# Kernel tuning notes

Hardware: AMD Instinct MI355X
Metric: run time of the kernel (lower is better)

Reference implementation:

```python
import jax, jax.numpy as jnp
import numpy as np

EMB_TABLE = 80000  # full shared embedding rows
N_ITEMS = 50000    # target item count (item_num + 1)
E = 600000         # edges
D = 128            # embedding_size
L = 3              # num_gcn_layers


def gcn_conv(x, W, b, src, dst, norm, n):
    # PyG GCNConv: x' = lin(x); out[i] = sum_{(j->i)} norm_ji * x'[j] + bias
    msgs = (x @ W)[src] * norm[:, None]          # [E+n, D]
    out = jax.ops.segment_sum(msgs, dst, num_segments=n)
    return out + b


def setup_inputs() -> dict:
    key = jax.random.key(0)
    k0, k1, k2 = jax.random.split(key, 3)
    item_emb = jax.random.normal(k0, (EMB_TABLE, D), dtype=jnp.float32) * 0.02
    weights = jax.random.normal(k1, (L, D, D), dtype=jnp.float32) * (1.0 / np.sqrt(D))
    biases = jnp.zeros((L, D), dtype=jnp.float32)
    edge_index = jax.random.randint(k2, (2, E), 0, N_ITEMS, dtype=jnp.int64)
    return {"item_emb": item_emb, "weights": weights, "biases": biases,
            "edge_index": edge_index, "item_nums": N_ITEMS}


def reference(item_emb, weights, biases, edge_index, item_nums):
    n = item_nums
    x0 = item_emb[-n:]  # embeds[0] = item_emb[-item_nums:]
    loops = jnp.arange(n, dtype=edge_index.dtype)
    src = jnp.concatenate([edge_index[0], loops])  # add self-loops (GCNConv default)
    dst = jnp.concatenate([edge_index[1], loops])
    # symmetric normalization: deg computed on target side with self-loops
    deg = jax.ops.segment_sum(jnp.ones_like(src, dtype=x0.dtype), dst, num_segments=n)
    dinv = jnp.where(deg > 0, jax.lax.rsqrt(jnp.maximum(deg, 1e-12)), 0.0)
    norm = dinv[src] * dinv[dst]                   # [E+n]
    embeds = [x0]
    for l in range(weights.shape[0]):
        embeds.append(gcn_conv(embeds[-1], weights[l], biases[l], src, dst, norm, n))
    total = embeds[0]
    for e in embeds[1:]:
        total = total + e
    return (total, *embeds)
```

## Files before the change

kernel.cpp:

```cpp
#include <hip/hip_runtime.h>
#include <stdint.h>

#define D 128

typedef unsigned int u32;
typedef unsigned short u16;

static __device__ __forceinline__ float bf2f(u16 h) {
    return __uint_as_float(((u32)h) << 16);
}
static __device__ __forceinline__ u16 f2bf(float f) {
    u32 u = __float_as_uint(f);
    u32 r = (u + 0x7fffu + ((u >> 16) & 1u)) >> 16;
    return (u16)r;
}
static __device__ __forceinline__ int clampi(int v, int n) {
    if (v < 0) v = 0;
    if (v >= n) v = n - 1;
    return v;
}

__global__ void k_init(int* __restrict__ hist, int* __restrict__ csr_pos, int n,
                       const u16* __restrict__ emb_raw, const u32* __restrict__ ei_raw,
                       const u16* __restrict__ w_raw, int* __restrict__ flags) {
    int i = blockIdx.x * 256 + threadIdx.x;
    if (i < n) {
        hist[i] = 0;
        csr_pos[i] = 0;
    }
    if (blockIdx.x == 0 && threadIdx.x < 64) {
        int t = threadIdx.x;
        int se = 0, sw = 0, zz = 0;
#pragma unroll
        for (int q = 0; q < 4; q++) {
            int k = t * 4 + q;
            u16 he = emb_raw[2 * k];
            u32 exe = (he >> 7) & 0xFF;
            if (he == 0 || (exe >= 0x60 && exe <= 0x8F)) se++;
            u16 hw = w_raw[2 * k];
            u32 exw = (hw >> 7) & 0xFF;
            if (hw == 0 || (exw >= 0x60 && exw <= 0x8F)) sw++;
            if (ei_raw[2 * k + 1] == 0) zz++;
        }
#pragma unroll
        for (int o = 32; o; o >>= 1) {
            se += __shfl_down(se, o);
            sw += __shfl_down(sw, o);
            zz += __shfl_down(zz, o);
        }
        if (t == 0) {
            flags[0] = (se >= 200) ? 1 : 0;
            flags[2] = (sw >= 200) ? 1 : 0;
            flags[1] = (zz >= 200) ? 1 : 0;
        }
    }
}

__global__ void k_hist(const u32* __restrict__ ei, int E, int n,
                       const int* __restrict__ flags, int* __restrict__ hist) {
    int e = blockIdx.x * 256 + threadIdx.x;
    if (e >= E) return;
    int d;
    if (flags[1]) d = ((const int2*)ei)[(size_t)E + e].x;
    else          d = (int)ei[(size_t)E + e];
    atomicAdd(&hist[clampi(d, n)], 1);
}

__global__ void k_scan1(const int* __restrict__ hist, int n,
                        int* __restrict__ incl, int* __restrict__ bsums) {
    __shared__ int s[256];
    int t = threadIdx.x;
    int i = blockIdx.x * 256 + t;
    int v = (i < n) ? hist[i] : 0;
    s[t] = v;
    __syncthreads();
    for (int d2 = 1; d2 < 256; d2 <<= 1) {
        int add = (t >= d2) ? s[t - d2] : 0;
        __syncthreads();
        s[t] += add;
        __syncthreads();
    }
    if (i < n) incl[i] = s[t];
    if (t == 255) bsums[blockIdx.x] = s[255];
}

__global__ void k_scan23(const int* __restrict__ hist, const int* __restrict__ bsums,
                         int n, int* __restrict__ csr_off, float* __restrict__ dinv) {
    __shared__ int s[256];
    int t = threadIdx.x, b = blockIdx.x;
    s[t] = (t < b) ? bsums[t] : 0;
    __syncthreads();
    for (int o = 128; o; o >>= 1) {
        if (t < o) s[t] += s[t + o];
        __syncthreads();
    }
    int add = s[0];
    int i = b * 256 + t;
    if (i < n) {
        int h = hist[i];
        csr_off[i] = add + csr_off[i] - h;
        dinv[i] = rsqrtf((float)(h + 1));
    }
}

__global__ void k_sx(const u32* __restrict__ ei, int E, int n,
                     const int* __restrict__ flags,
                     const int* __restrict__ csr_off, int* __restrict__ csr_pos,
                     const float* __restrict__ dinv, int2* __restrict__ csr_pair,
                     const void* __restrict__ emb, int off_elems, int nD4,
                     float* __restrict__ out_x0, int eb) {
    int bid = blockIdx.x;
    if (bid < eb) {
        int e = bid * 256 + threadIdx.x;
        if (e >= E) return;
        int s, d;
        if (flags[1]) {
            s = ((const int2*)ei)[e].x;
            d = ((const int2*)ei)[(size_t)E + e].x;
        } else {
            s = (int)ei[e];
            d = (int)ei[(size_t)E + e];
        }
        s = clampi(s, n);
        d = clampi(d, n);
        int p = csr_off[d] + atomicAdd(&csr_pos[d], 1);
        if (p >= E) p = E - 1;
        csr_pair[p] = make_int2(s, __float_as_int(dinv[s] * dinv[d]));
    } else {
        int i = (bid - eb) * 256 + threadIdx.x;
        if (i >= nD4) return;
        float4 v;
        if (flags[0]) {
            ushort4 h = ((const ushort4*)((const u16*)emb + off_elems))[i];
            v = make_float4(bf2f(h.x), bf2f(h.y), bf2f(h.z), bf2f(h.w));
        } else {
            v = ((const float4*)((const float*)emb + off_elems))[i];
        }
        ((float4*)out_x0)[i] = v;
    }
}

__global__ __launch_bounds__(256) void k_gemm(const float* __restrict__ A,
                                              const void* __restrict__ Wbase, int layer,
                                              const int* __restrict__ flags, int n,
                                              u32* __restrict__ Y) {
    __shared__ float Ws[D * D];
    int tid = threadIdx.x;
    const size_t woff = (size_t)layer * D * D;
    if (flags[2]) {
        const ushort4* w4 = (const ushort4*)((const u16*)Wbase + woff);
#pragma unroll
        for (int j = 0; j < 16; j++) {
            int e = j * 1024 + tid * 4;
            ushort4 h = w4[j * 256 + tid];
            Ws[e + 0] = bf2f(h.x);
            Ws[e + 1] = bf2f(h.y);
            Ws[e + 2] = bf2f(h.z);
            Ws[e + 3] = bf2f(h.w);
        }
    } else {
        const float4* w4 = (const float4*)((const float*)Wbase + woff);
#pragma unroll
        for (int j = 0; j < 16; j++) {
            int e = j * 1024 + tid * 4;
            float4 v = w4[j * 256 + tid];
            Ws[e + 0] = v.x;
            Ws[e + 1] = v.y;
            Ws[e + 2] = v.z;
            Ws[e + 3] = v.w;
        }
    }
    __syncthreads();

    int rowg = tid >> 4, colg = tid & 15;
    int row0 = blockIdx.x * 64 + rowg * 4;

    float acc[4][4][2];
#pragma unroll
    for (int r = 0; r < 4; r++)
#pragma unroll
        for (int j = 0; j < 4; j++) acc[r][j][0] = acc[r][j][1] = 0.0f;

    const float4* a4[4];
#pragma unroll
    for (int r = 0; r < 4; r++) {
        int rr = row0 + r;
        if (rr >= n) rr = 0;
        a4[r] = (const float4*)(A + (size_t)rr * D);
    }

    for (int kk = 0; kk < 32; kk++) {
        float av[4][4];
#pragma unroll
        for (int r = 0; r < 4; r++) {
            float4 t = a4[r][kk];
            av[r][0] = t.x; av[r][1] = t.y; av[r][2] = t.z; av[r][3] = t.w;
        }
#pragma unroll
        for (int e = 0; e < 4; e++) {
            int k = kk * 4 + e;
            float2 w[4];
#pragma unroll
            for (int j = 0; j < 4; j++)
                w[j] = *(const float2*)&Ws[k * D + 2 * colg + 32 * j];
#pragma unroll
            for (int r = 0; r < 4; r++)
#pragma unroll
                for (int j = 0; j < 4; j++) {
                    acc[r][j][0] += av[r][e] * w[j].x;
                    acc[r][j][1] += av[r][e] * w[j].y;
                }
        }
    }

#pragma unroll
    for (int r = 0; r < 4; r++) {
        int rr = row0 + r;
        if (rr < n) {
#pragma unroll
            for (int j = 0; j < 4; j++) {
                u32 pack = (u32)f2bf(acc[r][j][0]) | ((u32)f2bf(acc[r][j][1]) << 16);
                Y[(size_t)rr * 64 + colg + 16 * j] = pack;
            }
        }
    }
}

__global__ __launch_bounds__(256) void k_agg(const u32* __restrict__ Y,
                                             const int* __restrict__ csr_off,
                                             const int* __restrict__ cnt,
                                             const int2* __restrict__ csr_pair,
                                             const float* __restrict__ dinv,
                                             const void* __restrict__ bias_base, int layer,
                                             const int* __restrict__ flags, int n, int nD,
                                             const float* __restrict__ out_base,
                                             float* __restrict__ out_x,
                                             float* __restrict__ out_tot) {
    int i = blockIdx.x * 4 + (threadIdx.x >> 6);
    if (i >= n) return;
    int t = threadIdx.x & 63;

    float di = dinv[i];
    float di2 = di * di;
    u32 yv = Y[(size_t)i * 64 + t];
    float a0 = bf2f((u16)(yv & 0xffffu)) * di2;
    float a1 = bf2f((u16)(yv >> 16)) * di2;
    float c0 = 0.0f, c1 = 0.0f;

    int start = csr_off[i];
    int c = cnt[i];

    for (int base = 0; base < c; base += 64) {
        int m = c - base;
        if (m > 64) m = 64;
        int2 pr = (t < m) ? csr_pair[start + base + t] : make_int2(0, 0);
        int j = 0;
        for (; j + 3 < m; j += 4) {
            int s0 = __shfl(pr.x, j);
            int s1 = __shfl(pr.x, j + 1);
            int s2 = __shfl(pr.x, j + 2);
            int s3 = __shfl(pr.x, j + 3);
            float w0 = __uint_as_float((u32)__shfl(pr.y, j));
            float w1 = __uint_as_float((u32)__shfl(pr.y, j + 1));
            float w2 = __uint_as_float((u32)__shfl(pr.y, j + 2));
            float w3 = __uint_as_float((u32)__shfl(pr.y, j + 3));
            u32 v0 = Y[(size_t)s0 * 64 + t];
            u32 v1 = Y[(size_t)s1 * 64 + t];
            u32 v2 = Y[(size_t)s2 * 64 + t];
            u32 v3 = Y[(size_t)s3 * 64 + t];
            a0 += bf2f((u16)(v0 & 0xffffu)) * w0;
            a1 += bf2f((u16)(v0 >> 16)) * w0;
            c0 += bf2f((u16)(v1 & 0xffffu)) * w1;
            c1 += bf2f((u16)(v1 >> 16)) * w1;
            a0 += bf2f((u16)(v2 & 0xffffu)) * w2;
            a1 += bf2f((u16)(v2 >> 16)) * w2;
            c0 += bf2f((u16)(v3 & 0xffffu)) * w3;
            c1 += bf2f((u16)(v3 >> 16)) * w3;
        }
        for (; j < m; j++) {
            int s = __shfl(pr.x, j);
            float w = __uint_as_float((u32)__shfl(pr.y, j));
            u32 v = Y[(size_t)s * 64 + t];
            a0 += bf2f((u16)(v & 0xffffu)) * w;
            a1 += bf2f((u16)(v >> 16)) * w;
        }
    }
    float acc0 = a0 + c0, acc1 = a1 + c1;

    float b0, b1;
    if (flags[0]) {
        const u16* bb = (const u16*)bias_base + layer * D;
        b0 = bf2f(bb[2 * t]);
        b1 = bf2f(bb[2 * t + 1]);
    } else {
        const float* bb = (const float*)bias_base + layer * D;
        b0 = bb[2 * t];
        b1 = bb[2 * t + 1];
    }
    float xv0 = acc0 + b0, xv1 = acc1 + b1;
    size_t base = (size_t)i * D + 2 * t;
    *(float2*)&out_x[base] = make_float2(xv0, xv1);

    if (out_tot) {
        float2 s0 = *(const float2*)&out_base[(size_t)1 * nD + base];
        float2 s1 = *(const float2*)&out_base[(size_t)2 * nD + base];
        float2 s2 = *(const float2*)&out_base[(size_t)3 * nD + base];
        *(float2*)&out_tot[base] =
            make_float2(s0.x + s1.x + s2.x + xv0, s0.y + s1.y + s2.y + xv1);
    }
}

extern "C" void kernel_launch(void* const* d_in, const int* in_sizes, int n_in,
                              void* d_out, int out_size, void* d_ws, size_t ws_size,
                              hipStream_t stream) {
    float* out = (float*)d_out;

    const int n = out_size / (5 * D);

    int i_emb = -1, i_ei = -1, i_w = -1, i_b = -1;
    {
        int order[8];
        int m = n_in > 8 ? 8 : n_in;
        for (int i = 0; i < m; i++) order[i] = i;
        for (int a = 0; a < m; a++)
            for (int b2 = a + 1; b2 < m; b2++)
                if (in_sizes[order[b2]] > in_sizes[order[a]]) {
                    int tmp = order[a]; order[a] = order[b2]; order[b2] = tmp;
                }
        i_emb = order[0];
        i_ei  = (m > 1) ? order[1] : 0;
        for (int i = 0; i < m; i++) {
            if (in_sizes[i] == 3 * D * D && i_w < 0) i_w = i;
            if (in_sizes[i] == 3 * D && i_b < 0) i_b = i;
        }
        if (i_w < 0) i_w = (m > 2) ? order[2] : 0;
        if (i_b < 0) i_b = (m > 3) ? order[3] : 0;
    }
    const void* emb  = d_in[i_emb];
    const void* wts  = d_in[i_w];
    const void* bias = d_in[i_b];
    const u32*  ei   = (const u32*)d_in[i_ei];

    const int E = in_sizes[i_ei] / 2;
    const int rows = in_sizes[i_emb] / D;
    const int off_elems = (rows - n) * D;

    char* p = (char*)d_ws;
    auto take = [&](size_t bytes) {
        char* r = p;
        p += (bytes + 255) & ~(size_t)255;
        return r;
    };
    int*   flags    = (int*)  take(3 * 4);
    int*   hist     = (int*)  take((size_t)n * 4);
    int*   csr_pos  = (int*)  take((size_t)n * 4);
    int*   csr_off  = (int*)  take((size_t)n * 4);
    int*   bsums    = (int*)  take(256 * 4);
    float* dinv     = (float*)take((size_t)n * 4);
    int2*  csr_pair = (int2*) take((size_t)E * 8);
    u32*   ybuf     = (u32*)  take((size_t)n * 64 * 4);

    const int nD = n * D;
    const int nb = (n + 255) / 256;
    const int eb = (E + 255) / 256;
    const int x0b = (nD / 4 + 255) / 256;

    k_init<<<nb, 256, 0, stream>>>(hist, csr_pos, n, (const u16*)emb, ei,
                                   (const u16*)wts, flags);
    k_hist<<<eb, 256, 0, stream>>>(ei, E, n, flags, hist);
    k_scan1<<<nb, 256, 0, stream>>>(hist, n, csr_off, bsums);
    k_scan23<<<nb, 256, 0, stream>>>(hist, bsums, n, csr_off, dinv);
    k_sx<<<eb + x0b, 256, 0, stream>>>(ei, E, n, flags, csr_off, csr_pos, dinv,
                                       csr_pair, emb, off_elems, nD / 4,
                                       out + (size_t)nD, eb);

    const int ab = (n + 3) / 4;
    for (int l = 0; l < 3; l++) {
        const float* A = out + (size_t)(1 + l) * nD;
        float* ox = out + (size_t)(2 + l) * nD;
        k_gemm<<<(n + 63) / 64, 256, 0, stream>>>(A, wts, l, flags, n, ybuf);
        k_agg<<<ab, 256, 0, stream>>>(ybuf, csr_off, hist, csr_pair, dinv, bias, l,
                                      flags, n, nD, out, ox,
                                      (l == 2) ? out : (float*)nullptr);
    }
}
```

Measured before the change: 406.7 us.

## Use split-bf16 MFMA for the per-layer GEMM with prepacked weights

Replaces the scalar FP32 shared-memory GEMM with MFMA 16x16x32 bf16 instructions. Precision is kept close to fp32 by splitting both activations and weights into high and low bf16 parts and doing three MFMAs per tile. A new prep kernel converts and packs all three layers' weights into the MFMA operand layout once, so each GEMM block only copies them into LDS. The Y column layout changes from interleaved pairs to a c/c+64 split, and the aggregation kernel's bias and output indexing is adjusted to match, which gives up its float2 stores.

```diff
diff --git a/kernel.cpp b/kernel.cpp
--- a/kernel.cpp
+++ b/kernel.cpp
@@ -5,6 +5,8 @@
 
 typedef unsigned int u32;
 typedef unsigned short u16;
+typedef __attribute__((ext_vector_type(8))) short short8;
+typedef __attribute__((ext_vector_type(4))) float f32x4;
 
 static __device__ __forceinline__ float bf2f(u16 h) {
     return __uint_as_float(((u32)h) << 16);
@@ -54,6 +56,26 @@
             flags[1] = (zz >= 200) ? 1 : 0;
         }
     }
+}
+
+__global__ __launch_bounds__(256) void k_wprep(const void* __restrict__ Wbase,
+                                               const int* __restrict__ flags,
+                                               u16* __restrict__ WB) {
+    int idx = blockIdx.x * 256 + threadIdx.x;
+    int e = idx & 7;
+    int l = (idx >> 3) & 63;
+    int ks = (idx >> 9) & 3;
+    int c = (idx >> 11) & 7;
+    int layer = idx >> 14;
+    int k = ks * 32 + ((l >> 4) << 3) + e;
+    int j = (c << 4) + (l & 15);
+    size_t src = (size_t)layer * D * D + (size_t)k * D + j;
+    float w = flags[2] ? bf2f(((const u16*)Wbase)[src]) : ((const float*)Wbase)[src];
+    u16 hb = f2bf(w);
+    u16 lb = f2bf(w - bf2f(hb));
+    size_t o = (size_t)layer * 32768 + (size_t)((c * 4 + ks) * 64 + l) * 8 + e;
+    WB[o] = hb;
+    WB[o + 16384] = lb;
 }
 
 __global__ void k_hist(const u32* __restrict__ ei, int E, int n,
@@ -141,86 +163,58 @@
 }
 
 __global__ __launch_bounds__(256) void k_gemm(const float* __restrict__ A,
-                                              const void* __restrict__ Wbase, int layer,
-                                              const int* __restrict__ flags, int n,
-                                              u32* __restrict__ Y) {
-    __shared__ float Ws[D * D];
+                                              const u16* __restrict__ WB, int layer,
+                                              int n, u32* __restrict__ Y) {
+    __shared__ f32x4 ldsv[4096];
     int tid = threadIdx.x;
-    const size_t woff = (size_t)layer * D * D;
-    if (flags[2]) {
-        const ushort4* w4 = (const ushort4*)((const u16*)Wbase + woff);
-#pragma unroll
-        for (int j = 0; j < 16; j++) {
-            int e = j * 1024 + tid * 4;
-            ushort4 h = w4[j * 256 + tid];
-            Ws[e + 0] = bf2f(h.x);
-            Ws[e + 1] = bf2f(h.y);
-            Ws[e + 2] = bf2f(h.z);
-            Ws[e + 3] = bf2f(h.w);
-        }
-    } else {
-        const float4* w4 = (const float4*)((const float*)Wbase + woff);
-#pragma unroll
-        for (int j = 0; j < 16; j++) {
-            int e = j * 1024 + tid * 4;
-            float4 v = w4[j * 256 + tid];
-            Ws[e + 0] = v.x;
-            Ws[e + 1] = v.y;
-            Ws[e + 2] = v.z;
-            Ws[e + 3] = v.w;
-        }
+    {
+        const f32x4* src = (const f32x4*)(WB + (size_t)layer * 32768);
+#pragma unroll
+        for (int i = 0; i < 16; i++) ldsv[tid + 256 * i] = src[tid + 256 * i];
     }
     __syncthreads();
 
-    int rowg = tid >> 4, colg = tid & 15;
-    int row0 = blockIdx.x * 64 + rowg * 4;
-
-    float acc[4][4][2];
-#pragma unroll
-    for (int r = 0; r < 4; r++)
-#pragma unroll
-        for (int j = 0; j < 4; j++) acc[r][j][0] = acc[r][j][1] = 0.0f;
-
-    const float4* a4[4];
+    int w = tid >> 6, l = tid & 63;
+    int row0 = blockIdx.x * 64 + w * 16;
+    int ar = row0 + (l & 15);
+    if (ar >= n) ar = 0;
+    const float* Ab = A + (size_t)ar * D + ((l >> 4) << 3);
+
+    f32x4 acc[8] = {};
+    const short8* bp = (const short8*)ldsv;
+
+#pragma unroll
+    for (int ks = 0; ks < 4; ks++) {
+        f32x4 a0 = *(const f32x4*)(Ab + ks * 32);
+        f32x4 a1 = *(const f32x4*)(Ab + ks * 32 + 4);
+        float av[8] = {a0.x, a0.y, a0.z, a0.w, a1.x, a1.y, a1.z, a1.w};
+        short8 ah, al;
+#pragma unroll
+        for (int e = 0; e < 8; e++) {
+            u16 h = f2bf(av[e]);
+            ah[e] = (short)h;
+            al[e] = (short)f2bf(av[e] - bf2f(h));
+        }
+#pragma unroll
+        for (int c = 0; c < 8; c++) {
+            short8 bh = bp[(c * 4 + ks) * 64 + l];
+            short8 bl = bp[2048 + (c * 4 + ks) * 64 + l];
+            acc[c] = __builtin_amdgcn_mfma_f32_16x16x32_bf16(al, bh, acc[c], 0, 0, 0);
+            acc[c] = __builtin_amdgcn_mfma_f32_16x16x32_bf16(ah, bl, acc[c], 0, 0, 0);
+            acc[c] = __builtin_amdgcn_mfma_f32_16x16x32_bf16(ah, bh, acc[c], 0, 0, 0);
+        }
+    }
+
+    int rbase = row0 + ((l >> 4) << 2);
+    int col = l & 15;
 #pragma unroll
     for (int r = 0; r < 4; r++) {
-        int rr = row0 + r;
-        if (rr >= n) rr = 0;
-        a4[r] = (const float4*)(A + (size_t)rr * D);
-    }
-
-    for (int kk = 0; kk < 32; kk++) {
-        float av[4][4];
-#pragma unroll
-        for (int r = 0; r < 4; r++) {
-            float4 t = a4[r][kk];
-            av[r][0] = t.x; av[r][1] = t.y; av[r][2] = t.z; av[r][3] = t.w;
-        }
-#pragma unroll
-        for (int e = 0; e < 4; e++) {
-            int k = kk * 4 + e;
-            float2 w[4];
-#pragma unroll
-            for (int j = 0; j < 4; j++)
-                w[j] = *(const float2*)&Ws[k * D + 2 * colg + 32 * j];
-#pragma unroll
-            for (int r = 0; r < 4; r++)
-#pragma unroll
-                for (int j = 0; j < 4; j++) {
-                    acc[r][j][0] += av[r][e] * w[j].x;
-                    acc[r][j][1] += av[r][e] * w[j].y;
-                }
-        }
-    }
-
-#pragma unroll
-    for (int r = 0; r < 4; r++) {
-        int rr = row0 + r;
-        if (rr < n) {
-#pragma unroll
-            for (int j = 0; j < 4; j++) {
-                u32 pack = (u32)f2bf(acc[r][j][0]) | ((u32)f2bf(acc[r][j][1]) << 16);
-                Y[(size_t)rr * 64 + colg + 16 * j] = pack;
+        int gr = rbase + r;
+        if (gr < n) {
+#pragma unroll
+            for (int c = 0; c < 4; c++) {
+                u32 pack = (u32)f2bf(acc[c][r]) | ((u32)f2bf(acc[c + 4][r]) << 16);
+                Y[(size_t)gr * 64 + c * 16 + col] = pack;
             }
         }
     }
@@ -290,23 +284,25 @@
     float b0, b1;
     if (flags[0]) {
         const u16* bb = (const u16*)bias_base + layer * D;
-        b0 = bf2f(bb[2 * t]);
-        b1 = bf2f(bb[2 * t + 1]);
+        b0 = bf2f(bb[t]);
+        b1 = bf2f(bb[t + 64]);
     } else {
         const float* bb = (const float*)bias_base + layer * D;
-        b0 = bb[2 * t];
-        b1 = bb[2 * t + 1];
+        b0 = bb[t];
+        b1 = bb[t + 64];
     }
     float xv0 = acc0 + b0, xv1 = acc1 + b1;
-    size_t base = (size_t)i * D + 2 * t;
-    *(float2*)&out_x[base] = make_float2(xv0, xv1);
+    size_t base = (size_t)i * D + t;
+    out_x[base] = xv0;
+    out_x[base + 64] = xv1;
 
     if (out_tot) {
-        float2 s0 = *(const float2*)&out_base[(size_t)1 * nD + base];
-        float2 s1 = *(const float2*)&out_base[(size_t)2 * nD + base];
-        float2 s2 = *(const float2*)&out_base[(size_t)3 * nD + base];
-        *(float2*)&out_tot[base] =
-            make_float2(s0.x + s1.x + s2.x + xv0, s0.y + s1.y + s2.y + xv1);
+        float s0 = out_base[(size_t)1 * nD + base] + out_base[(size_t)2 * nD + base] +
+                   out_base[(size_t)3 * nD + base];
+        float s1 = out_base[(size_t)1 * nD + base + 64] + out_base[(size_t)2 * nD + base + 64] +
+                   out_base[(size_t)3 * nD + base + 64];
+        out_tot[base] = s0 + xv0;
+        out_tot[base + 64] = s1 + xv1;
     }
 }
 
@@ -359,6 +355,7 @@
     float* dinv     = (float*)take((size_t)n * 4);
     int2*  csr_pair = (int2*) take((size_t)E * 8);
     u32*   ybuf     = (u32*)  take((size_t)n * 64 * 4);
+    u16*   wb       = (u16*)  take((size_t)3 * 32768 * 2);
 
     const int nD = n * D;
     const int nb = (n + 255) / 256;
@@ -367,6 +364,7 @@
 
     k_init<<<nb, 256, 0, stream>>>(hist, csr_pos, n, (const u16*)emb, ei,
                                    (const u16*)wts, flags);
+    k_wprep<<<192, 256, 0, stream>>>(wts, flags, wb);
     k_hist<<<eb, 256, 0, stream>>>(ei, E, n, flags, hist);
     k_scan1<<<nb, 256, 0, stream>>>(hist, n, csr_off, bsums);
     k_scan23<<<nb, 256, 0, stream>>>(hist, bsums, n, csr_off, dinv);
@@ -378,7 +376,7 @@
     for (int l = 0; l < 3; l++) {
         const float* A = out + (size_t)(1 + l) * nD;
         float* ox = out + (size_t)(2 + l) * nD;
-        k_gemm<<<(n + 63) / 64, 256, 0, stream>>>(A, wts, l, flags, n, ybuf);
+        k_gemm<<<(n + 63) / 64, 256, 0, stream>>>(A, wb, l, n, ybuf);
         k_agg<<<ab, 256, 0, stream>>>(ybuf, csr_off, hist, csr_pair, dinv, bias, l,
                                       flags, n, nD, out, ox,
                                       (l == 2) ? out : (float*)nullptr);
```

Result: faster. 353.6 us (-13.1%).
